# Performance work log

Hardware: AMD Instinct MI355X
Metric: run time of the kernel (lower is better)

The kernel has to match this reference:

```python
import jax, jax.numpy as jnp
import numpy as np

B, C, H, W = 4, 64, 64, 64
CI = C // 2  # inter_channels


def setup_inputs() -> dict:
    key = jax.random.key(0)
    k1, k2, k3, k4, k5 = jax.random.split(key, 5)
    x = jax.random.normal(k1, (B, C, H, W), dtype=jnp.float32)
    # 1x1 conv g: in C -> CI (weight [CI, C], bias [CI])
    Wg = jax.random.normal(k2, (CI, C), dtype=jnp.float32) * (1.0 / np.sqrt(C))
    bg = jax.random.normal(k3, (CI,), dtype=jnp.float32) * 0.01
    # 1x1 conv W_z: CI -> C
    Wz = jax.random.normal(k4, (C, CI), dtype=jnp.float32) * (1.0 / np.sqrt(CI))
    bz = jax.random.normal(k5, (C,), dtype=jnp.float32) * 0.01
    return {"x": x, "Wg": Wg, "bg": bg, "Wz": Wz, "bz": bz}


def reference(x, Wg, bg, Wz, bz):
    b, c, h, w = x.shape
    n = h * w
    xf = x.reshape(b, c, n)                       # [B,C,N]
    # g projection (1x1 conv) then flatten: [B,N,CI]
    g_x = jnp.einsum('bcn,oc->bno', xf, Wg) + bg  # [B,N,CI]
    # theta = phi = raw x flattened
    theta = xf.transpose(0, 2, 1)                 # [B,N,C]
    f = jnp.einsum('bnc,bcm->bnm', theta, xf)     # [B,N,N]
    f_div_C = jax.nn.softmax(f, axis=-1)
    y = jnp.einsum('bnm,bmo->bno', f_div_C, g_x)  # [B,N,CI]
    y = y.transpose(0, 2, 1).reshape(b, CI, h, w)  # [B,CI,H,W]
    # W_z projection (1x1 conv) + residual
    W_y = jnp.einsum('oi,bihw->bohw', Wz, y) + bz[None, :, None, None]
    return W_y + x
```

## Files before the change

### kernel.cpp

```cpp
#include <hip/hip_runtime.h>
#include <hip/hip_bf16.h>
#include <math.h>

#define B_  4
#define C_  64
#define N_  4096
#define CI_ 32

typedef __attribute__((ext_vector_type(8))) unsigned short u16x8;
typedef __attribute__((ext_vector_type(8))) __bf16        bf16x8;
typedef __attribute__((ext_vector_type(4))) __bf16        bf16x4;
typedef __attribute__((ext_vector_type(4))) float         f32x4;

__device__ __forceinline__ unsigned short f2bf(float f) {
    union { float f; unsigned int i; } v; v.f = f;
    unsigned int r = v.i + 0x7FFFu + ((v.i >> 16) & 1u);
    return (unsigned short)(r >> 16);
}

__global__ __launch_bounds__(256) void k_prep(
    const float* __restrict__ x, const float* __restrict__ Wg,
    const float* __restrict__ bg, unsigned short* __restrict__ xT,
    unsigned short* __restrict__ gx, float* __restrict__ diag)
{
    __shared__ __align__(16) float tile[64][68];
    __shared__ float part[4][64][33];
    const int t  = threadIdx.x;
    const int b  = blockIdx.x >> 6;
    const int n0 = (blockIdx.x & 63) * 64;

    #pragma unroll
    for (int pass = 0; pass < 4; ++pass) {
        int c   = (t >> 4) + pass * 16;
        int nl4 = (t & 15) * 4;
        float4 v = *(const float4*)(x + (size_t)(b * C_ + c) * N_ + n0 + nl4);
        *(float4*)&tile[c][nl4] = v;
    }
    __syncthreads();

    {
        const int n  = t >> 2;
        const int cc = (t & 3) * 16;
        u16x8 a, b2;
        #pragma unroll
        for (int j = 0; j < 8; ++j) a[j]  = f2bf(tile[cc + j][n]);
        #pragma unroll
        for (int j = 0; j < 8; ++j) b2[j] = f2bf(tile[cc + 8 + j][n]);
        unsigned short* dst = xT + (size_t)(b * N_ + n0 + n) * C_ + cc;
        *(u16x8*)dst       = a;
        *(u16x8*)(dst + 8) = b2;
    }
    {
        const int nl = t & 63, cq = t >> 6;
        float acc[CI_];
        #pragma unroll
        for (int o = 0; o < CI_; ++o) acc[o] = 0.f;
        float dd = 0.f;
        #pragma unroll 4
        for (int cl = 0; cl < 16; ++cl) {
            int c = cq * 16 + cl;
            float xv = tile[c][nl];
            dd += xv * xv;
            #pragma unroll
            for (int o = 0; o < CI_; ++o) acc[o] += Wg[o * C_ + c] * xv;
        }
        #pragma unroll
        for (int o = 0; o < CI_; ++o) part[cq][nl][o] = acc[o];
        part[cq][nl][32] = dd;
    }
    __syncthreads();
    {
        const int o = t >> 3, nr = (t & 7) * 8;
        u16x8 w;
        #pragma unroll
        for (int j = 0; j < 8; ++j) {
            int n = nr + j;
            float s = part[0][n][o] + part[1][n][o] + part[2][n][o] + part[3][n][o]
                    + bg[o];
            w[j] = f2bf(s);
        }
        *(u16x8*)(gx + (size_t)(b * CI_ + o) * N_ + n0 + nr) = w;
    }
    if (t < 64)
        diag[(size_t)b * N_ + n0 + t] =
            part[0][t][32] + part[1][t][32] + part[2][t][32] + part[3][t][32];
}

__device__ __forceinline__ f32x4 mfma16(bf16x8 a, bf16x8 b, f32x4 c) {
    return __builtin_amdgcn_mfma_f32_16x16x32_bf16(a, b, c, 0, 0, 0);
}

#define KLOAD(kr, tT)                                                          \
    kr[0] = *(const u16x8*)(kSrc0 + (size_t)(tT) * (32 * C_));                 \
    kr[1] = *(const u16x8*)(kSrc1 + (size_t)(tT) * (32 * C_));

#define KSTORE(bufS, kr)                                                       \
    *(u16x8*)((bufS) + kDst0) = kr[0];                                         \
    *(u16x8*)((bufS) + kDst1) = kr[1];

#define VLOAD(vr, tT)                                                          \
    vr[0] = *(const bf16x8*)(bBase0 + (tT) * 32);                              \
    vr[1] = *(const bf16x8*)(bBase1 + (tT) * 32);

#define COMPUTE(ABUF, Vr)                                                      \
    {                                                                          \
        bf16x8 Af[2][2];                                                       \
        _Pragma("unroll")                                                      \
        for (int kt = 0; kt < 2; ++kt) {                                       \
            _Pragma("unroll")                                                  \
            for (int kc = 0; kc < 2; ++kc)                                     \
                Af[kt][kc] = *(const bf16x8*)((ABUF)                           \
                    + (g * 32 + kt * 16 + li) * 72 + kc * 32 + quad * 8);      \
        }                                                                      \
        f32x4 S[2][2];                                                         \
        _Pragma("unroll")                                                      \
        for (int kt = 0; kt < 2; ++kt) {                                       \
            _Pragma("unroll")                                                  \
            for (int qt = 0; qt < 2; ++qt) {                                   \
                f32x4 z = (f32x4){nKq[qt], nKq[qt], nKq[qt], nKq[qt]};         \
                z = mfma16(Af[kt][0], Qf[qt][0], z);                           \
                S[kt][qt] = mfma16(Af[kt][1], Qf[qt][1], z);                   \
            }                                                                  \
        }                                                                      \
        _Pragma("unroll")                                                      \
        for (int qt = 0; qt < 2; ++qt) {                                       \
            _Pragma("unroll")                                                  \
            for (int kt = 0; kt < 2; ++kt) {                                   \
                bf16x4 pb;                                                     \
                _Pragma("unroll")                                              \
                for (int r = 0; r < 4; ++r) {                                  \
                    float p = __expf(S[kt][qt][r]);                            \
                    lacc[qt] += p;                                             \
                    pb[r] = (__bf16)p;                                         \
                }                                                              \
                *(bf16x4*)(pW + qt * 640 + kt * 16) = pb;                      \
            }                                                                  \
        }                                                                      \
        bf16x8 Ap[2];                                                          \
        _Pragma("unroll")                                                      \
        for (int qt = 0; qt < 2; ++qt)                                         \
            Ap[qt] = *(const bf16x8*)(pR + qt * 640);                          \
        _Pragma("unroll")                                                      \
        for (int qt = 0; qt < 2; ++qt) {                                       \
            _Pragma("unroll")                                                  \
            for (int ot = 0; ot < 2; ++ot)                                     \
                Yf[qt][ot] = mfma16(Ap[qt], Vr[ot], Yf[qt][ot]);               \
        }                                                                      \
    }

__global__ __launch_bounds__(256, 4) void k_flash(
    const unsigned short* __restrict__ xT, const unsigned short* __restrict__ gx,
    const float* __restrict__ diag,
    float* __restrict__ ypart, float* __restrict__ lpart)
{
    __shared__ __align__(16) char smem[28672];
    unsigned short* xk0 = (unsigned short*)smem;
    unsigned short* xk1 = (unsigned short*)(smem + 9216);
    unsigned short* Pl  = (unsigned short*)(smem + 18432);

    const int tid  = threadIdx.x;
    const int wave = tid >> 6, lane = tid & 63;
    const int quad = lane >> 4, li = lane & 15;
    const int g = wave >> 1, qh = wave & 1;
    const int bi    = blockIdx.x;
    const int xcd   = bi & 7;
    const int combo = xcd * 2 + ((bi >> 3) & 1);
    const int b     = combo >> 2;
    const int kq    = combo & 3;
    const int qtb   = bi >> 4;
    const int qw  = qtb * 64 + qh * 32;
    const int u   = tid & 127;

    const unsigned short* xb = xT + (size_t)b * N_ * C_;
    const unsigned short* gb = gx + (size_t)b * CI_ * N_;

    float nKq[2];
    #pragma unroll
    for (int qt = 0; qt < 2; ++qt)
        nKq[qt] = -diag[(size_t)b * N_ + qw + qt * 16 + li];

    bf16x8 Qf[2][2];
    #pragma unroll
    for (int qt = 0; qt < 2; ++qt)
        #pragma unroll
        for (int kc = 0; kc < 2; ++kc)
            Qf[qt][kc] = *(const bf16x8*)(xb + (size_t)(qw + qt * 16 + li) * C_
                                          + kc * 32 + quad * 8);

    f32x4 Yf[2][2];
    #pragma unroll
    for (int qt = 0; qt < 2; ++qt)
        #pragma unroll
        for (int ot = 0; ot < 2; ++ot)
            Yf[qt][ot] = (f32x4){0.f, 0.f, 0.f, 0.f};
    float lacc[2] = {0.f, 0.f};

    const int keybase = kq * 1024 + g * 512;
    const int gg = tid >> 7;
    const int sbase = kq * 1024 + gg * 512;

    const int cc0 = u * 2,      key0 = cc0 >> 3, cof0 = (cc0 & 7) * 8;
    const int cc1 = u * 2 + 1,  key1 = cc1 >> 3, cof1 = (cc1 & 7) * 8;
    const unsigned short* kSrc0 = xb + (size_t)(sbase + key0) * C_ + cof0;
    const unsigned short* kSrc1 = xb + (size_t)(sbase + key1) * C_ + cof1;
    const int kDst0 = (gg * 32 + key0) * 72 + cof0;
    const int kDst1 = (gg * 32 + key1) * 72 + cof1;

    const unsigned short* bBase0 = gb + (size_t)(li) * N_      + keybase + quad * 8;
    const unsigned short* bBase1 = gb + (size_t)(16 + li) * N_ + keybase + quad * 8;

    unsigned short*       pW = Pl + (wave * 32 + li) * 40 + quad * 4;
    const unsigned short* pR = Pl + (wave * 32 + li) * 40 + quad * 8;

    u16x8  kA[2], kB[2];
    bf16x8 vA[2], vB[2];
    KLOAD(kA, 0) VLOAD(vA, 0)
    KLOAD(kB, 1) VLOAD(vB, 1)
    KSTORE(xk0, kA)
    KLOAD(kA, 2)
    __syncthreads();

    #pragma unroll 1
    for (int t2 = 0; t2 < 8; ++t2) {
        const int te = 2 * t2;
        KSTORE(xk1, kB)
        COMPUTE(xk0, vA)
        { const int nk = (te + 3 < 16) ? te + 3 : 15; KLOAD(kB, nk) }
        { const int nv = (te + 2 < 16) ? te + 2 : 15; VLOAD(vA, nv) }
        __syncthreads();
        if (t2 < 7) { KSTORE(xk0, kA) }
        COMPUTE(xk1, vB)
        { const int nk = (te + 4 < 16) ? te + 4 : 15; KLOAD(kA, nk) }
        { const int nv = (te + 3 < 16) ? te + 3 : 15; VLOAD(vB, nv) }
        __syncthreads();
    }

    #pragma unroll
    for (int qt = 0; qt < 2; ++qt) {
        lacc[qt] += __shfl_xor(lacc[qt], 16, 64);
        lacc[qt] += __shfl_xor(lacc[qt], 32, 64);
    }

    float* ym = (float*)smem;

    #pragma unroll
    for (int qt = 0; qt < 2; ++qt) {
        #pragma unroll
        for (int ot = 0; ot < 2; ++ot)
            #pragma unroll
            for (int r = 0; r < 4; ++r)
                ym[(wave * 32 + qt * 16 + quad * 4 + r) * 34 + ot * 16 + li] = Yf[qt][ot][r];
        if (quad == 0)
            ym[(wave * 32 + qt * 16 + li) * 34 + 32] = lacc[qt];
    }
    __syncthreads();
    {
        const int q = tid >> 2, og = tid & 3;
        const int qh2 = q >> 5, ql = q & 31;
        const int w0 = qh2, w1 = 2 + qh2;
        const size_t pbase = (size_t)(b * 64 + qtb) * 4 + kq;
        float* yp = ypart + pbase * 2048 + q * 32;
        #pragma unroll
        for (int j = 0; j < 8; ++j) {
            int o = og * 8 + j;
            yp[o] = ym[(w0 * 32 + ql) * 34 + o] + ym[(w1 * 32 + ql) * 34 + o];
        }
        if (og == 0)
            lpart[pbase * 64 + q] = ym[(w0 * 32 + ql) * 34 + 32]
                                  + ym[(w1 * 32 + ql) * 34 + 32];
    }
}

__global__ __launch_bounds__(256) void k_merge(
    const float* __restrict__ ypart, const float* __restrict__ lpart,
    const float* __restrict__ x, const float* __restrict__ Wz,
    const float* __restrict__ bz, float* __restrict__ out)
{
    __shared__ float yfin[64][33];
    const int t   = threadIdx.x;
    const int b   = blockIdx.x >> 6;
    const int qtb = blockIdx.x & 63;
    const int q0  = qtb * 64;

    {
        const int q = t >> 2, og = t & 3;
        const size_t pb = (size_t)(b * 64 + qtb) * 4;
        float l = lpart[(pb + 0) * 64 + q] + lpart[(pb + 1) * 64 + q]
                + lpart[(pb + 2) * 64 + q] + lpart[(pb + 3) * 64 + q];
        float inv = 1.f / l;
        #pragma unroll
        for (int j = 0; j < 8; ++j) {
            int o = og * 8 + j;
            float acc = 0.f;
            #pragma unroll
            for (int kq = 0; kq < 4; ++kq)
                acc += ypart[(pb + kq) * 2048 + q * 32 + o];
            yfin[q][o] = acc * inv;
        }
    }
    __syncthreads();
    {
        const int q = t & 63, c0 = t >> 6;
        #pragma unroll
        for (int i = 0; i < 16; ++i) {
            int cout = c0 + i * 4;
            float acc = bz[cout];
            #pragma unroll
            for (int o = 0; o < CI_; ++o)
                acc += Wz[cout * CI_ + o] * yfin[q][o];
            size_t oidx = (size_t)(b * C_ + cout) * N_ + q0 + q;
            out[oidx] = acc + x[oidx];
        }
    }
}

extern "C" void kernel_launch(void* const* d_in, const int* in_sizes, int n_in,
                              void* d_out, int out_size, void* d_ws, size_t ws_size,
                              hipStream_t stream) {
    (void)in_sizes; (void)n_in; (void)out_size; (void)ws_size;
    const float* x  = (const float*)d_in[0];
    const float* Wg = (const float*)d_in[1];
    const float* bg = (const float*)d_in[2];
    const float* Wz = (const float*)d_in[3];
    const float* bz = (const float*)d_in[4];
    float* out = (float*)d_out;

    unsigned short* xT = (unsigned short*)d_ws;
    unsigned short* gx = (unsigned short*)((char*)d_ws + 2097152);
    float* diag  = (float*)((char*)d_ws + 3145728);
    float* ypart = (float*)((char*)d_ws + 3211264);
    float* lpart = (float*)((char*)d_ws + 11599872);

    hipLaunchKernelGGL(k_prep,  dim3(B_ * (N_ / 64)),    dim3(256), 0, stream, x, Wg, bg, xT, gx, diag);
    hipLaunchKernelGGL(k_flash, dim3(B_ * 64 * 4),       dim3(256), 0, stream, xT, gx, diag, ypart, lpart);
    hipLaunchKernelGGL(k_merge, dim3(B_ * 64),           dim3(256), 0, stream, ypart, lpart, x, Wz, bz, out);
}
```

Before: 111.1 us.

## Software-pipeline QK/exp and PV phases with double-buffered P tile

Splits the per-tile compute into a QK^T+exp phase and a P·V phase, and double-buffers the P staging area in shared memory. The PV step for one tile is now deferred and interleaved with the QK step of the next tile, so the LDS write/read dependency on P no longer stalls within a single tile. V loads are rescheduled to match, and a final PV runs after the loop. This adds about 10 KB of shared memory per block, which may reduce occupancy, and adds a barrier before the epilogue reuses shared memory.

```diff
diff --git a/kernel.cpp b/kernel.cpp
--- a/kernel.cpp
+++ b/kernel.cpp
@@ -102,7 +102,7 @@
     vr[0] = *(const bf16x8*)(bBase0 + (tT) * 32);                              \
     vr[1] = *(const bf16x8*)(bBase1 + (tT) * 32);
 
-#define COMPUTE(ABUF, Vr)                                                      \
+#define QKPH(ABUF, PWp)                                                        \
     {                                                                          \
         bf16x8 Af[2][2];                                                       \
         _Pragma("unroll")                                                      \
@@ -133,13 +133,17 @@
                     lacc[qt] += p;                                             \
                     pb[r] = (__bf16)p;                                         \
                 }                                                              \
-                *(bf16x4*)(pW + qt * 640 + kt * 16) = pb;                      \
+                *(bf16x4*)((PWp) + qt * 640 + kt * 16) = pb;                   \
             }                                                                  \
         }                                                                      \
+    }
+
+#define PVPH(PRp, Vr)                                                          \
+    {                                                                          \
         bf16x8 Ap[2];                                                          \
         _Pragma("unroll")                                                      \
         for (int qt = 0; qt < 2; ++qt)                                         \
-            Ap[qt] = *(const bf16x8*)(pR + qt * 640);                          \
+            Ap[qt] = *(const bf16x8*)((PRp) + qt * 640);                       \
         _Pragma("unroll")                                                      \
         for (int qt = 0; qt < 2; ++qt) {                                       \
             _Pragma("unroll")                                                  \
@@ -153,10 +157,11 @@
     const float* __restrict__ diag,
     float* __restrict__ ypart, float* __restrict__ lpart)
 {
-    __shared__ __align__(16) char smem[28672];
+    __shared__ __align__(16) char smem[38912];
     unsigned short* xk0 = (unsigned short*)smem;
     unsigned short* xk1 = (unsigned short*)(smem + 9216);
-    unsigned short* Pl  = (unsigned short*)(smem + 18432);
+    unsigned short* Pl0 = (unsigned short*)(smem + 18432);
+    unsigned short* Pl1 = (unsigned short*)(smem + 28672);
 
     const int tid  = threadIdx.x;
     const int wave = tid >> 6, lane = tid & 63;
@@ -209,13 +214,15 @@
     const unsigned short* bBase0 = gb + (size_t)(li) * N_      + keybase + quad * 8;
     const unsigned short* bBase1 = gb + (size_t)(16 + li) * N_ + keybase + quad * 8;
 
-    unsigned short*       pW = Pl + (wave * 32 + li) * 40 + quad * 4;
-    const unsigned short* pR = Pl + (wave * 32 + li) * 40 + quad * 8;
+    unsigned short*       pW0 = Pl0 + (wave * 32 + li) * 40 + quad * 4;
+    const unsigned short* pR0 = Pl0 + (wave * 32 + li) * 40 + quad * 8;
+    unsigned short*       pW1 = Pl1 + (wave * 32 + li) * 40 + quad * 4;
+    const unsigned short* pR1 = Pl1 + (wave * 32 + li) * 40 + quad * 8;
 
     u16x8  kA[2], kB[2];
     bf16x8 vA[2], vB[2];
     KLOAD(kA, 0) VLOAD(vA, 0)
-    KLOAD(kB, 1) VLOAD(vB, 1)
+    KLOAD(kB, 1)
     KSTORE(xk0, kA)
     KLOAD(kA, 2)
     __syncthreads();
@@ -224,16 +231,19 @@
     for (int t2 = 0; t2 < 8; ++t2) {
         const int te = 2 * t2;
         KSTORE(xk1, kB)
-        COMPUTE(xk0, vA)
+        QKPH(xk0, pW0)
+        if (t2 > 0) { PVPH(pR1, vB) }
         { const int nk = (te + 3 < 16) ? te + 3 : 15; KLOAD(kB, nk) }
+        VLOAD(vB, te + 1)
+        __syncthreads();
+        if (t2 < 7) { KSTORE(xk0, kA) }
+        QKPH(xk1, pW1)
+        PVPH(pR0, vA)
+        { const int nk = (te + 4 < 16) ? te + 4 : 15; KLOAD(kA, nk) }
         { const int nv = (te + 2 < 16) ? te + 2 : 15; VLOAD(vA, nv) }
         __syncthreads();
-        if (t2 < 7) { KSTORE(xk0, kA) }
-        COMPUTE(xk1, vB)
-        { const int nk = (te + 4 < 16) ? te + 4 : 15; KLOAD(kA, nk) }
-        { const int nv = (te + 3 < 16) ? te + 3 : 15; VLOAD(vB, nv) }
-        __syncthreads();
-    }
+    }
+    PVPH(pR1, vB)
 
     #pragma unroll
     for (int qt = 0; qt < 2; ++qt) {
@@ -241,6 +251,7 @@
         lacc[qt] += __shfl_xor(lacc[qt], 32, 64);
     }
 
+    __syncthreads();
     float* ym = (float*)smem;
 
     #pragma unroll
```

New measurement: 110.9 us. Within noise of the previous version (-0.1%).
